# Performance work log

Measured on AMD Instinct MI355X. Metric: run time of the kernel, lower is better.

## Reference

```python
import jax, jax.numpy as jnp
import numpy as np

WP = 1.0     # warp_penalty
TEMP = 0.01  # soft-min temperature
BIG = 1e7    # finite stand-in for +inf (exp(-BIG/TEMP) == 0 exactly in fp32)


def setup_inputs() -> dict:
    key = jax.random.key(0)
    k1, k2, k3, k4 = jax.random.split(key, 4)
    B, T1, T2, C = 8, 256, 1024, 128
    fea_a = jax.random.normal(k1, (B, T1, C), jnp.float32)
    fea_b = jax.random.normal(k2, (B, T2, C), jnp.float32)
    len_a = jax.random.randint(k3, (B,), T1 // 2, T1 + 1)
    len_b = jax.random.randint(k4, (B,), T2 // 2, T2 + 1)
    return {"fea_a": fea_a, "len_a": len_a, "fea_b": fea_b, "len_b": len_b}


def _softmin(v, temp):
    # v: [3, B, T1]; stable -temp*log(sum(exp(-v/temp)))
    m = jnp.min(v, axis=0)
    return m - temp * jnp.log(jnp.sum(jnp.exp(-(v - m) / temp), axis=0))


def _soft_dtw(fea_a, fea_b, len_a, len_b, wp=WP, temp=TEMP):
    B, T1, C = fea_a.shape
    T2 = fea_b.shape[1]
    # L1 cost: [B, T2, T1]  (rows index fea_b, cols index fea_a, as in torch code)
    cost = jnp.mean(jnp.abs(fea_a[:, None, :, :] - fea_b[:, :, None, :]), axis=-1)
    # skewed cost: skew[b, d, j] = cost[b, clip(d-j, 0, T2-1), j]
    D = T1 + T2 - 1
    d = jnp.arange(D)[:, None]
    j = jnp.arange(T1)[None, :]
    idx = jnp.clip(d - j, 0, T2 - 1)           # [D, T1]
    skew = cost[:, idx, j]                      # [B, D, T1]
    skew = jnp.swapaxes(skew, 0, 1)             # [D, B, T1] for scan

    pc0 = jnp.full((B, T1 + 1), BIG, jnp.float32)       # path_cost (diag d-1)
    pcp0 = pc0.at[:, 0].set(0.0)                         # path_cost_prev (diag d-2)

    def step(carry, crow):
        pc, pcp = carry
        dirs = jnp.stack([pcp[:, :-1], pc[:, 1:] + wp, pc[:, :-1] + wp], axis=0)
        new = crow + _softmin(dirs, temp)                # [B, T1]
        new = jnp.concatenate([jnp.full((B, 1), BIG, new.dtype), new], axis=1)
        return (new, pc), new

    _, ys = jax.lax.scan(step, (pc0, pcp0), skew)        # ys: [D, B, T1+1]
    # per-sample answer: diagonal len_a+len_b-2, entry len_a
    di = len_a + len_b - 2
    loss_i = ys[di, jnp.arange(B), len_a]
    return jnp.sum(loss_i)  # reduction='mean' over a length-1 accumulator == sum


def reference(fea_a, len_a, fea_b, len_b):
    return _soft_dtw(fea_a, fea_b, len_a, len_b)
```

## Files before the change

### kernel.cpp

```cpp
#include <hip/hip_runtime.h>
#include <hip/hip_bf16.h>
#include <hip/hip_fp16.h>
#include <cstddef>
#include <cstdint>

#define BIGV 10000000.0f
#define WPV  1.0f

#define BATCH 8
#define T1N 256
#define T2N 1024
#define CN 128
#define DN 1279

#define FLAG_MAGIC 0x600D0000

typedef __attribute__((ext_vector_type(2))) _Float16 half2v;

__global__ __launch_bounds__(256) void cost_kernel(const float* __restrict__ A,
                                                   const float* __restrict__ Bf,
                                                   const int* __restrict__ lenA,
                                                   const int* __restrict__ lenB,
                                                   float* __restrict__ sk) {
    __shared__ char As[64 * 256];
    __shared__ char Bs[127 * 256];

    const int b  = blockIdx.z;
    const int d0 = blockIdx.y * 64;
    const int j0 = blockIdx.x * 64;
    const int tid = threadIdx.x;

    const int dEnd = lenA[b] + lenB[b] - 2;
    if (d0 > dEnd) return;

    const float* Ab = A  + (size_t)b * T1N * CN;
    const float* Bb = Bf + (size_t)b * T2N * CN;

    const int tj = tid & 15;
    const int td = tid >> 4;
    const int brow0 = td - tj + 63;
    const int rbase = d0 - j0 - 63;

#define SWB(row, g) (((row) << 8) + ((((g) + (row)) & 15) << 4))

    #pragma unroll
    for (int i = 0; i < 8; ++i) {
        int idx = tid + i * 256;
        int row = idx >> 5;
        int q   = idx & 31;
        float4 f = *(const float4*)(Ab + (size_t)(j0 + row) * CN + (q << 2));
        half2v h0 = { (_Float16)f.x, (_Float16)f.y };
        half2v h1 = { (_Float16)f.z, (_Float16)f.w };
        char* dst = As + SWB(row, q >> 1) + ((q & 1) << 3);
        ((uint32_t*)dst)[0] = __builtin_bit_cast(uint32_t, h0);
        ((uint32_t*)dst)[1] = __builtin_bit_cast(uint32_t, h1);
    }
    #pragma unroll
    for (int i = 0; i < 16; ++i) {
        int idx = tid + i * 256;
        if (idx < 4064) {
            int row = idx >> 5;
            int q   = idx & 31;
            int gr = rbase + row;
            gr = gr < 0 ? 0 : (gr > T2N - 1 ? T2N - 1 : gr);
            float4 f = *(const float4*)(Bb + (size_t)gr * CN + (q << 2));
            half2v h0 = { (_Float16)f.x, (_Float16)f.y };
            half2v h1 = { (_Float16)f.z, (_Float16)f.w };
            char* dst = Bs + SWB(row, q >> 1) + ((q & 1) << 3);
            ((uint32_t*)dst)[0] = __builtin_bit_cast(uint32_t, h0);
            ((uint32_t*)dst)[1] = __builtin_bit_cast(uint32_t, h1);
        }
    }
    __syncthreads();

    float acc[4][4];
    #pragma unroll
    for (int i = 0; i < 4; ++i)
        #pragma unroll
        for (int j = 0; j < 4; ++j) acc[i][j] = 0.0f;

    const half2v one2 = { (_Float16)1.0f, (_Float16)1.0f };

    for (int g = 0; g < 16; ++g) {
        uint4 a4[4], bv[7];
        #pragma unroll
        for (int ji = 0; ji < 4; ++ji) {
            int row = tj + 16 * ji;
            a4[ji] = *(const uint4*)(As + SWB(row, g));
        }
        #pragma unroll
        for (int m = 0; m < 7; ++m) {
            int row = brow0 + 16 * (m - 3);
            bv[m] = *(const uint4*)(Bs + SWB(row, g));
        }
        #pragma unroll
        for (int dk = 0; dk < 4; ++dk) {
            #pragma unroll
            for (int ji = 0; ji < 4; ++ji) {
                uint4 au = a4[ji];
                uint4 bu = bv[dk - ji + 3];
                float a = acc[dk][ji];
                #pragma unroll
                for (int w = 0; w < 4; ++w) {
                    uint32_t ua = (&au.x)[w];
                    uint32_t ub = (&bu.x)[w];
                    half2v d2 = __builtin_bit_cast(half2v, ua)
                              - __builtin_bit_cast(half2v, ub);
                    uint32_t du = __builtin_bit_cast(uint32_t, d2) & 0x7FFF7FFFu;
#if __has_builtin(__builtin_amdgcn_fdot2)
                    a = __builtin_amdgcn_fdot2(__builtin_bit_cast(half2v, du),
                                               one2, a, false);
#else
                    half2v ad = __builtin_bit_cast(half2v, du);
                    a += (float)ad.x + (float)ad.y;
#endif
                }
                acc[dk][ji] = a;
            }
        }
    }
#undef SWB

    #pragma unroll
    for (int dk = 0; dk < 4; ++dk) {
        int d = d0 + td + 16 * dk;
        if (d < DN) {
            size_t rowoff = ((size_t)b * DN + d) * T1N;
            #pragma unroll
            for (int ji = 0; ji < 4; ++ji) {
                int j = j0 + tj + 16 * ji;
                sk[rowoff + j] = acc[dk][ji] * (1.0f / 128.0f);
            }
        }
    }
}

__device__ __forceinline__ float min3f(float a, float b, float c) {
    float d;
    asm("v_min3_f32 %0, %1, %2, %3" : "=v"(d) : "v"(a), "v"(b), "v"(c));
    return d;
}

__global__ __launch_bounds__(64, 1) void dp_reg3_kernel(const float* __restrict__ sk,
                                                        const int* __restrict__ lenA,
                                                        const int* __restrict__ lenB,
                                                        float* __restrict__ partials,
                                                        int* __restrict__ flags,
                                                        float* __restrict__ out) {
    const int b = blockIdx.x;
    const int L = threadIdx.x;

    const int la = __builtin_amdgcn_readfirstlane(lenA[b]);
    const int lb = __builtin_amdgcn_readfirstlane(lenB[b]);
    const int dEnd = la + lb - 2;
    const int kLast = dEnd >> 4;

    const char* base = (const char*)(sk + (size_t)b * DN * T1N);
    const int lo = L << 4;

    float x0 = BIGV, x1 = BIGV, x2 = BIGV, x3 = BIGV;
    float y0 = BIGV, y1 = BIGV, y2 = BIGV, y3 = BIGV;
    float pp = (L == 0) ? 0.0f : BIGV;

    float4 A0, A1, A2, A3, A4c, A5, A6, A7, A8, A9, A10, A11, A12, A13, A14, A15;
    float4 B0, B1, B2, B3, B4c, B5, B6, B7, B8, B9, B10, B11, B12, B13, B14, B15;
    float4 C0, C1, C2, C3, C4c, C5, C6, C7, C8, C9, C10, C11, C12, C13, C14, C15;

#define SHFL_UP1(SRC)                                                       \
    __int_as_float(__builtin_amdgcn_update_dpp(                             \
        __float_as_int(BIGV), __float_as_int(SRC),                          \
        0x138 , 0xF, 0xF, false))

#define LOAD1(DST, KB, R)                                                   \
        DST = *(const float4*)(base + (((KB) << 14) + ((R) << 10)) + lo)

#define LOADALL(P, KB) do {                                                 \
        LOAD1(P##0, KB, 0);   LOAD1(P##1, KB, 1);   LOAD1(P##2, KB, 2);     \
        LOAD1(P##3, KB, 3);   LOAD1(P##4c, KB, 4);  LOAD1(P##5, KB, 5);     \
        LOAD1(P##6, KB, 6);   LOAD1(P##7, KB, 7);   LOAD1(P##8, KB, 8);     \
        LOAD1(P##9, KB, 9);   LOAD1(P##10, KB, 10); LOAD1(P##11, KB, 11);   \
        LOAD1(P##12, KB, 12); LOAD1(P##13, KB, 13); LOAD1(P##14, KB, 14);   \
        LOAD1(P##15, KB, 15);                                               \
    } while (0)

#define DPP_STEP(C4, P, Q) do {                                             \
        float4 c_ = (C4);                                                   \
        float p1_ = SHFL_UP1(P##3);                                         \
        float w0_ = P##0 + WPV, w1_ = P##1 + WPV;                           \
        float w2_ = P##2 + WPV, w3_ = P##3 + WPV;                           \
        float wp_ = p1_ + WPV;                                              \
        float t0_ = c_.x + min3f(pp, w0_, wp_);                             \
        float t1_ = c_.y + min3f(Q##0, w1_, w0_);                           \
        float t2_ = c_.z + min3f(Q##1, w2_, w1_);                           \
        float t3_ = c_.w + min3f(Q##2, w3_, w2_);                           \
        pp = p1_;                                                           \
        Q##0 = t0_; Q##1 = t1_; Q##2 = t2_; Q##3 = t3_;                     \
    } while (0)

#define PROC_FULL(P) do {                                                   \
        DPP_STEP(P##0,  x, y); DPP_STEP(P##1,  y, x);                       \
        DPP_STEP(P##2,  x, y); DPP_STEP(P##3,  y, x);                       \
        DPP_STEP(P##4c, x, y); DPP_STEP(P##5,  y, x);                       \
        DPP_STEP(P##6,  x, y); DPP_STEP(P##7,  y, x);                       \
        DPP_STEP(P##8,  x, y); DPP_STEP(P##9,  y, x);                       \
        DPP_STEP(P##10, x, y); DPP_STEP(P##11, y, x);                       \
        DPP_STEP(P##12, x, y); DPP_STEP(P##13, y, x);                       \
        DPP_STEP(P##14, x, y); DPP_STEP(P##15, y, x);                       \
    } while (0)

#define GSTEP(C4, PN, QN, R) do { if ((R) <= rem) DPP_STEP(C4, PN, QN); } while (0)
#define PROC_GUARD(P) do {                                                  \
        GSTEP(P##0,  x, y, 0);  GSTEP(P##1,  y, x, 1);                      \
        GSTEP(P##2,  x, y, 2);  GSTEP(P##3,  y, x, 3);                      \
        GSTEP(P##4c, x, y, 4);  GSTEP(P##5,  y, x, 5);                      \
        GSTEP(P##6,  x, y, 6);  GSTEP(P##7,  y, x, 7);                      \
        GSTEP(P##8,  x, y, 8);  GSTEP(P##9,  y, x, 9);                      \
        GSTEP(P##10, x, y, 10); GSTEP(P##11, y, x, 11);                     \
        GSTEP(P##12, x, y, 12); GSTEP(P##13, y, x, 13);                     \
        GSTEP(P##14, x, y, 14); GSTEP(P##15, y, x, 15);                     \
    } while (0)

    LOADALL(A, 0);
    LOADALL(B, 1);
    LOADALL(C, 2);

    int k = 0;
    while (k + 2 < kLast) {
        PROC_FULL(A);
        if (k + 3 <= kLast) LOADALL(A, k + 3);
        PROC_FULL(B);
        if (k + 4 <= kLast) LOADALL(B, k + 4);
        PROC_FULL(C);
        if (k + 5 <= kLast) LOADALL(C, k + 5);
        k += 3;
    }

    const int rem = dEnd & 15;
    if (kLast - k == 2)      { PROC_FULL(A); PROC_FULL(B); PROC_GUARD(C); }
    else if (kLast - k == 1) { PROC_FULL(A); PROC_GUARD(B); }
    else                     { PROC_GUARD(A); }

    float f0, f1, f2, f3;
    if ((rem & 1) == 0) { f0 = y0; f1 = y1; f2 = y2; f3 = y3; }
    else                { f0 = x0; f1 = x1; f2 = x2; f3 = x3; }

    const int tcap = la - 1;
    if (L == (tcap >> 2)) {
        const int kk = tcap & 3;
        float r = f0;
        if (kk == 1) r = f1;
        else if (kk == 2) r = f2;
        else if (kk == 3) r = f3;
        partials[b] = r;
        __threadfence();
        __hip_atomic_store(&flags[b], FLAG_MAGIC + b,
                           __ATOMIC_RELEASE, __HIP_MEMORY_SCOPE_AGENT);
    }

    if (b == 0 && L == 0) {
        float s = 0.0f;
        for (int i = 0; i < BATCH; ++i) {
            while (__hip_atomic_load(&flags[i], __ATOMIC_ACQUIRE,
                                     __HIP_MEMORY_SCOPE_AGENT) != FLAG_MAGIC + i)
                __builtin_amdgcn_s_sleep(2);
            s += __hip_atomic_load(&partials[i], __ATOMIC_RELAXED,
                                   __HIP_MEMORY_SCOPE_AGENT);
        }
        out[0] = s;
    }
#undef PROC_GUARD
#undef GSTEP
#undef PROC_FULL
#undef DPP_STEP
#undef LOADALL
#undef LOAD1
#undef SHFL_UP1
}

extern "C" void kernel_launch(void* const* d_in, const int* in_sizes, int n_in,
                              void* d_out, int out_size, void* d_ws, size_t ws_size,
                              hipStream_t stream) {
    const float* feaA = (const float*)d_in[0];
    const int*   lenA = (const int*)d_in[1];
    const float* feaB = (const float*)d_in[2];
    const int*   lenB = (const int*)d_in[3];

    float* sk       = (float*)d_ws;
    float* partials = (float*)((char*)d_ws + (size_t)BATCH * DN * T1N * sizeof(float));
    int*   flags    = (int*)(partials + BATCH);

    cost_kernel<<<dim3(T1N / 64, (DN + 63) / 64, BATCH), 256, 0, stream>>>(feaA, feaB, lenA, lenB, sk);
    dp_reg3_kernel<<<BATCH, 64, 0, stream>>>(sk, lenA, lenB, partials, flags, (float*)d_out);
}
```

Baseline: 131.8 us.

## Stream DP cost tiles through an LDS ring via async global-to-LDS loads

Replaces the three-deep register prefetch of skewed cost rows in the serial DP kernel with a three-slot LDS ring buffer. Rows are fetched by direct global-to-LDS loads with explicit vmcnt waits and read back into registers just before compute. This is meant to cut VGPR pressure and keep more loads in flight during the serial anti-diagonal recurrence. In exchange it adds LDS round-trips and hand-written waitcnt synchronization that depends on exact per-lane load counts. The tail handling also assumes at least three blocks are processed before the guarded final block.

```diff
diff --git a/kernel.cpp b/kernel.cpp
--- a/kernel.cpp
+++ b/kernel.cpp
@@ -141,12 +141,14 @@
     return d;
 }
 
-__global__ __launch_bounds__(64, 1) void dp_reg3_kernel(const float* __restrict__ sk,
-                                                        const int* __restrict__ lenA,
-                                                        const int* __restrict__ lenB,
-                                                        float* __restrict__ partials,
-                                                        int* __restrict__ flags,
-                                                        float* __restrict__ out) {
+__global__ __launch_bounds__(64, 1) void dp_lds_kernel(const float* __restrict__ sk,
+                                                       const int* __restrict__ lenA,
+                                                       const int* __restrict__ lenB,
+                                                       float* __restrict__ partials,
+                                                       int* __restrict__ flags,
+                                                       float* __restrict__ out) {
+    __shared__ char ring[3 * 16384];
+
     const int b = blockIdx.x;
     const int L = threadIdx.x;
 
@@ -155,33 +157,60 @@
     const int dEnd = la + lb - 2;
     const int kLast = dEnd >> 4;
 
-    const char* base = (const char*)(sk + (size_t)b * DN * T1N);
-    const int lo = L << 4;
+    const float* skb = sk + (size_t)b * DN * T1N + (L << 2);
+
+    char* s0 = ring;
+    char* s1 = ring + 16384;
+    char* s2 = ring + 32768;
 
     float x0 = BIGV, x1 = BIGV, x2 = BIGV, x3 = BIGV;
     float y0 = BIGV, y1 = BIGV, y2 = BIGV, y3 = BIGV;
     float pp = (L == 0) ? 0.0f : BIGV;
-
-    float4 A0, A1, A2, A3, A4c, A5, A6, A7, A8, A9, A10, A11, A12, A13, A14, A15;
-    float4 B0, B1, B2, B3, B4c, B5, B6, B7, B8, B9, B10, B11, B12, B13, B14, B15;
-    float4 C0, C1, C2, C3, C4c, C5, C6, C7, C8, C9, C10, C11, C12, C13, C14, C15;
 
 #define SHFL_UP1(SRC)                                                       \
     __int_as_float(__builtin_amdgcn_update_dpp(                             \
         __float_as_int(BIGV), __float_as_int(SRC),                          \
         0x138 , 0xF, 0xF, false))
 
-#define LOAD1(DST, KB, R)                                                   \
-        DST = *(const float4*)(base + (((KB) << 14) + ((R) << 10)) + lo)
-
-#define LOADALL(P, KB) do {                                                 \
-        LOAD1(P##0, KB, 0);   LOAD1(P##1, KB, 1);   LOAD1(P##2, KB, 2);     \
-        LOAD1(P##3, KB, 3);   LOAD1(P##4c, KB, 4);  LOAD1(P##5, KB, 5);     \
-        LOAD1(P##6, KB, 6);   LOAD1(P##7, KB, 7);   LOAD1(P##8, KB, 8);     \
-        LOAD1(P##9, KB, 9);   LOAD1(P##10, KB, 10); LOAD1(P##11, KB, 11);   \
-        LOAD1(P##12, KB, 12); LOAD1(P##13, KB, 13); LOAD1(P##14, KB, 14);   \
-        LOAD1(P##15, KB, 15);                                               \
-    } while (0)
+#define WAITV(N) do {                                                       \
+        asm volatile("s_waitcnt vmcnt(" #N ")" ::: "memory");               \
+        __builtin_amdgcn_sched_barrier(0);                                  \
+    } while (0)
+
+#define WAITL0 do {                                                         \
+        asm volatile("s_waitcnt lgkmcnt(0)" ::: "memory");                  \
+        __builtin_amdgcn_sched_barrier(0);                                  \
+    } while (0)
+
+#define ISSUE(KB, SL) do {                                                  \
+        _Pragma("unroll")                                                   \
+        for (int r_ = 0; r_ < 16; ++r_) {                                   \
+            int row_ = ((KB) << 4) + r_;                                    \
+            row_ = row_ > DN - 1 ? DN - 1 : row_;                           \
+            __builtin_amdgcn_global_load_lds(                               \
+                (const __attribute__((address_space(1))) void*)(skb + (size_t)row_ * T1N), \
+                (__attribute__((address_space(3))) void*)((SL) + (r_ << 10)), \
+                16, 0, 0);                                                  \
+        }                                                                   \
+    } while (0)
+
+#define READ16(SL)                                                          \
+        float4 cc0  = *(const float4*)((SL) +  0 * 1024 + (L << 4));        \
+        float4 cc1  = *(const float4*)((SL) +  1 * 1024 + (L << 4));        \
+        float4 cc2  = *(const float4*)((SL) +  2 * 1024 + (L << 4));        \
+        float4 cc3  = *(const float4*)((SL) +  3 * 1024 + (L << 4));        \
+        float4 cc4  = *(const float4*)((SL) +  4 * 1024 + (L << 4));        \
+        float4 cc5  = *(const float4*)((SL) +  5 * 1024 + (L << 4));        \
+        float4 cc6  = *(const float4*)((SL) +  6 * 1024 + (L << 4));        \
+        float4 cc7  = *(const float4*)((SL) +  7 * 1024 + (L << 4));        \
+        float4 cc8  = *(const float4*)((SL) +  8 * 1024 + (L << 4));        \
+        float4 cc9  = *(const float4*)((SL) +  9 * 1024 + (L << 4));        \
+        float4 cc10 = *(const float4*)((SL) + 10 * 1024 + (L << 4));        \
+        float4 cc11 = *(const float4*)((SL) + 11 * 1024 + (L << 4));        \
+        float4 cc12 = *(const float4*)((SL) + 12 * 1024 + (L << 4));        \
+        float4 cc13 = *(const float4*)((SL) + 13 * 1024 + (L << 4));        \
+        float4 cc14 = *(const float4*)((SL) + 14 * 1024 + (L << 4));        \
+        float4 cc15 = *(const float4*)((SL) + 15 * 1024 + (L << 4));
 
 #define DPP_STEP(C4, P, Q) do {                                             \
         float4 c_ = (C4);                                                   \
@@ -197,48 +226,63 @@
         Q##0 = t0_; Q##1 = t1_; Q##2 = t2_; Q##3 = t3_;                     \
     } while (0)
 
-#define PROC_FULL(P) do {                                                   \
-        DPP_STEP(P##0,  x, y); DPP_STEP(P##1,  y, x);                       \
-        DPP_STEP(P##2,  x, y); DPP_STEP(P##3,  y, x);                       \
-        DPP_STEP(P##4c, x, y); DPP_STEP(P##5,  y, x);                       \
-        DPP_STEP(P##6,  x, y); DPP_STEP(P##7,  y, x);                       \
-        DPP_STEP(P##8,  x, y); DPP_STEP(P##9,  y, x);                       \
-        DPP_STEP(P##10, x, y); DPP_STEP(P##11, y, x);                       \
-        DPP_STEP(P##12, x, y); DPP_STEP(P##13, y, x);                       \
-        DPP_STEP(P##14, x, y); DPP_STEP(P##15, y, x);                       \
+#define COMPUTE16 do {                                                      \
+        DPP_STEP(cc0,  x, y); DPP_STEP(cc1,  y, x);                         \
+        DPP_STEP(cc2,  x, y); DPP_STEP(cc3,  y, x);                         \
+        DPP_STEP(cc4,  x, y); DPP_STEP(cc5,  y, x);                         \
+        DPP_STEP(cc6,  x, y); DPP_STEP(cc7,  y, x);                         \
+        DPP_STEP(cc8,  x, y); DPP_STEP(cc9,  y, x);                         \
+        DPP_STEP(cc10, x, y); DPP_STEP(cc11, y, x);                         \
+        DPP_STEP(cc12, x, y); DPP_STEP(cc13, y, x);                         \
+        DPP_STEP(cc14, x, y); DPP_STEP(cc15, y, x);                         \
     } while (0)
 
 #define GSTEP(C4, PN, QN, R) do { if ((R) <= rem) DPP_STEP(C4, PN, QN); } while (0)
-#define PROC_GUARD(P) do {                                                  \
-        GSTEP(P##0,  x, y, 0);  GSTEP(P##1,  y, x, 1);                      \
-        GSTEP(P##2,  x, y, 2);  GSTEP(P##3,  y, x, 3);                      \
-        GSTEP(P##4c, x, y, 4);  GSTEP(P##5,  y, x, 5);                      \
-        GSTEP(P##6,  x, y, 6);  GSTEP(P##7,  y, x, 7);                      \
-        GSTEP(P##8,  x, y, 8);  GSTEP(P##9,  y, x, 9);                      \
-        GSTEP(P##10, x, y, 10); GSTEP(P##11, y, x, 11);                     \
-        GSTEP(P##12, x, y, 12); GSTEP(P##13, y, x, 13);                     \
-        GSTEP(P##14, x, y, 14); GSTEP(P##15, y, x, 15);                     \
-    } while (0)
-
-    LOADALL(A, 0);
-    LOADALL(B, 1);
-    LOADALL(C, 2);
+#define GUARD16 do {                                                        \
+        GSTEP(cc0,  x, y, 0);  GSTEP(cc1,  y, x, 1);                        \
+        GSTEP(cc2,  x, y, 2);  GSTEP(cc3,  y, x, 3);                        \
+        GSTEP(cc4,  x, y, 4);  GSTEP(cc5,  y, x, 5);                        \
+        GSTEP(cc6,  x, y, 6);  GSTEP(cc7,  y, x, 7);                        \
+        GSTEP(cc8,  x, y, 8);  GSTEP(cc9,  y, x, 9);                        \
+        GSTEP(cc10, x, y, 10); GSTEP(cc11, y, x, 11);                       \
+        GSTEP(cc12, x, y, 12); GSTEP(cc13, y, x, 13);                       \
+        GSTEP(cc14, x, y, 14); GSTEP(cc15, y, x, 15);                       \
+    } while (0)
+
+    ISSUE(0, s0);
+    ISSUE(1, s1);
+    ISSUE(2, s2);
 
     int k = 0;
-    while (k + 2 < kLast) {
-        PROC_FULL(A);
-        if (k + 3 <= kLast) LOADALL(A, k + 3);
-        PROC_FULL(B);
-        if (k + 4 <= kLast) LOADALL(B, k + 4);
-        PROC_FULL(C);
-        if (k + 5 <= kLast) LOADALL(C, k + 5);
-        k += 3;
-    }
-
+    for (; k + 2 < kLast; ++k) {
+        WAITV(32);
+        READ16(s0);
+        WAITL0;
+        ISSUE(k + 3, s0);
+        COMPUTE16;
+        { char* t_ = s0; s0 = s1; s1 = s2; s2 = t_; }
+    }
+
+    {
+        WAITV(32);
+        READ16(s0);
+        WAITL0;
+        COMPUTE16;
+        { char* t_ = s0; s0 = s1; s1 = s2; s2 = t_; }
+    }
+    {
+        WAITV(16);
+        READ16(s0);
+        WAITL0;
+        COMPUTE16;
+        { char* t_ = s0; s0 = s1; s1 = s2; s2 = t_; }
+    }
     const int rem = dEnd & 15;
-    if (kLast - k == 2)      { PROC_FULL(A); PROC_FULL(B); PROC_GUARD(C); }
-    else if (kLast - k == 1) { PROC_FULL(A); PROC_GUARD(B); }
-    else                     { PROC_GUARD(A); }
+    {
+        WAITV(0);
+        READ16(s0);
+        GUARD16;
+    }
 
     float f0, f1, f2, f3;
     if ((rem & 1) == 0) { f0 = y0; f1 = y1; f2 = y2; f3 = y3; }
@@ -268,12 +312,14 @@
         }
         out[0] = s;
     }
-#undef PROC_GUARD
+#undef GUARD16
 #undef GSTEP
-#undef PROC_FULL
+#undef COMPUTE16
 #undef DPP_STEP
-#undef LOADALL
-#undef LOAD1
+#undef READ16
+#undef ISSUE
+#undef WAITL0
+#undef WAITV
 #undef SHFL_UP1
 }
 
@@ -290,5 +336,5 @@
     int*   flags    = (int*)(partials + BATCH);
 
     cost_kernel<<<dim3(T1N / 64, (DN + 63) / 64, BATCH), 256, 0, stream>>>(feaA, feaB, lenA, lenB, sk);
-    dp_reg3_kernel<<<BATCH, 64, 0, stream>>>(sk, lenA, lenB, partials, flags, (float*)d_out);
+    dp_lds_kernel<<<BATCH, 64, 0, stream>>>(sk, lenA, lenB, partials, flags, (float*)d_out);
 }
```

Result: slower. 143.0 us (+8.5%).
